# Optimization experiments

Measured on AMD Instinct MI355X. Metric: run time of the kernel, lower is better.

The kernel has to match this reference:

```python
import jax, jax.numpy as jnp
import numpy as np

B, S, IN_DIM = 8, 2048, 8
EMB, HEADS, NCLS = 512, 8, 3
HDIM = EMB // HEADS
HALF = EMB // 2


def setup_inputs() -> dict:
    key = jax.random.key(0)
    ks = jax.random.split(key, 16)
    g = lambda k, shp, fan_in: jax.random.normal(k, shp, jnp.float32) / np.sqrt(fan_in)
    return {
        "features": jax.random.normal(ks[0], (B, S, IN_DIM), jnp.float32),
        "timestamps": jax.random.uniform(ks[1], (B, S, 1), jnp.float32),
        # FeatureEmbedding
        "Wf": g(ks[2], (IN_DIM, EMB), IN_DIM), "bf": jnp.zeros((EMB,), jnp.float32),
        # Time2Vec
        "Wl": g(ks[3], (1, HALF), 1), "bl": jnp.zeros((HALF,), jnp.float32),
        "Wp": g(ks[4], (1, HALF), 1), "bp": jnp.zeros((HALF,), jnp.float32),
        # TimeAwareAttention
        "Wq": g(ks[5], (EMB, EMB), EMB), "bq": jnp.zeros((EMB,), jnp.float32),
        "Wk": g(ks[6], (EMB, EMB), EMB), "bk": jnp.zeros((EMB,), jnp.float32),
        "Wv": g(ks[7], (EMB, EMB), EMB), "bv": jnp.zeros((EMB,), jnp.float32),
        "Wo": g(ks[8], (EMB, EMB), EMB), "bo": jnp.zeros((EMB,), jnp.float32),
        "time_decay": jnp.ones((1,), jnp.float32),
        # Classifier MLP (dropout is identity in eval)
        "W1": g(ks[9], (EMB, EMB // 2), EMB), "b1": jnp.zeros((EMB // 2,), jnp.float32),
        "W2": g(ks[10], (EMB // 2, NCLS), EMB // 2), "b2": jnp.zeros((NCLS,), jnp.float32),
    }


def reference(features, timestamps, Wf, bf, Wl, bl, Wp, bp,
              Wq, bq, Wk, bk, Wv, bv, Wo, bo, time_decay, W1, b1, W2, b2):
    # embeddings: feature linear + Time2Vec(linear || sin(linear))
    feat_emb = features @ Wf + bf                              # [B,S,E]
    time_emb = jnp.concatenate(
        [timestamps @ Wl + bl, jnp.sin(timestamps @ Wp + bp)], axis=-1)
    x = feat_emb + time_emb                                    # [B,S,E]

    # pairwise time-decay weights: exp(-decay * |t_i - t_j|)  [B,S,S]
    t = timestamps[..., 0]
    decay = jnp.exp(-time_decay[0] * jnp.abs(t[:, :, None] - t[:, None, :]))

    def split_heads(y):  # [B,S,E] -> [B,H,S,D]
        return y.reshape(B, S, HEADS, HDIM).transpose(0, 2, 1, 3)

    q = split_heads(x @ Wq + bq)
    k = split_heads(x @ Wk + bk)
    v = split_heads(x @ Wv + bv)

    scores = jnp.einsum('bhsd,bhtd->bhst', q, k) / np.sqrt(HDIM).astype(np.float32)
    scores = scores * decay[:, None, :, :]                     # elementwise decay bias
    attn = jax.nn.softmax(scores, axis=-1)
    out = jnp.einsum('bhst,bhtd->bhsd', attn, v)               # [B,H,S,D]
    out = out.transpose(0, 2, 1, 3).reshape(B, S, EMB)
    out = out @ Wo + bo

    h = out[:, -1, :]                                          # last token
    h = jax.nn.relu(h @ W1 + b1)
    logits = h @ W2 + b2                                       # [B,NCLS]
    return logits
```

## Files before the change

### kernel.cpp

```cpp
#include <hip/hip_runtime.h>
#include <hip/hip_bf16.h>
#include <math.h>

#define B 8
#define S 2048
#define IN_DIM 8
#define EMB 512
#define HEADS 8
#define HDIM 64
#define HALF 256
#define NCLS 3
#define NCHUNK 64
#define CT 32

#define WS_KQ    0
#define WS_COEF1 32768
#define WS_PM    33536
#define WS_PS    99072
#define WS_POP   1147648

__global__ __launch_bounds__(256) void k_head(
    const float* __restrict__ feat, const float* __restrict__ ts,
    const float* __restrict__ Wf, const float* __restrict__ bf,
    const float* __restrict__ Wl, const float* __restrict__ bl,
    const float* __restrict__ Wp, const float* __restrict__ bp,
    const float* __restrict__ Wq, const float* __restrict__ bq,
    const float* __restrict__ Wk, const float* __restrict__ bk,
    float* __restrict__ ws)
{
    const int h = blockIdx.x;
    const int b = blockIdx.y;
    const int bh = b*HEADS + h;
    const int tid = threadIdx.x;
    __shared__ float xl[EMB];
    __shared__ __align__(16) float qc[HDIM];
    __shared__ float kq[EMB];
    __shared__ float red[4][64];
    __shared__ float red10[4][12];

    {
        const float tl = ts[b*S + (S-1)];
        float fv[IN_DIM];
        #pragma unroll
        for (int i = 0; i < IN_DIM; ++i) fv[i] = feat[(b*S + (S-1))*IN_DIM + i];
        #pragma unroll
        for (int r = 0; r < 2; ++r) {
            const int e = tid + r*256;
            float acc = bf[e];
            #pragma unroll
            for (int i = 0; i < IN_DIM; ++i) acc += fv[i]*Wf[i*EMB + e];
            if (r == 0) acc += tl*Wl[e] + bl[e];
            else        acc += __sinf(tl*Wp[e-HALF] + bp[e-HALF]);
            xl[e] = acc;
        }
    }
    __syncthreads();
    {
        const int eo = tid & 63, jq = tid >> 6;
        float acc = (jq == 0) ? bq[h*HDIM + eo] : 0.f;
        #pragma unroll 8
        for (int j = jq*128; j < jq*128 + 128; ++j)
            acc += xl[j]*Wq[j*EMB + h*HDIM + eo];
        red[jq][eo] = acc;
    }
    __syncthreads();
    if (tid < HDIM) qc[tid] = red[0][tid]+red[1][tid]+red[2][tid]+red[3][tid];
    __syncthreads();
    {
        #pragma unroll
        for (int r = 0; r < 2; ++r) {
            const int j = tid + r*256;
            const float4* wr = (const float4*)(Wk + j*EMB + h*HDIM);
            const float4* qv = (const float4*)qc;
            float acc = 0.f;
            #pragma unroll
            for (int k = 0; k < 16; ++k) {
                const float4 w = wr[k], q4 = qv[k];
                acc += w.x*q4.x + w.y*q4.y + w.z*q4.z + w.w*q4.w;
            }
            kq[j] = acc;
            if (j >= HALF) ws[WS_KQ + bh*EMB + j] = acc;
        }
    }
    __syncthreads();
    {
        float a[IN_DIM] = {0.f,0.f,0.f,0.f,0.f,0.f,0.f,0.f};
        float c0 = 0.f, c1 = 0.f;
        #pragma unroll
        for (int r = 0; r < 2; ++r) {
            const int e = tid + r*256;
            const float kv = kq[e];
            #pragma unroll
            for (int i = 0; i < IN_DIM; ++i) a[i] += Wf[i*EMB + e]*kv;
            c0 += bf[e]*kv;
            if (r == 0) { c0 += bl[e]*kv; c1 += Wl[e]*kv; }
        }
        if (tid < HDIM) c0 += qc[tid]*bk[h*HDIM + tid];
        #pragma unroll
        for (int off = 32; off >= 1; off >>= 1) {
            #pragma unroll
            for (int i = 0; i < IN_DIM; ++i) a[i] += __shfl_xor(a[i], off, 64);
            c0 += __shfl_xor(c0, off, 64);
            c1 += __shfl_xor(c1, off, 64);
        }
        const int wid = tid >> 6, lane = tid & 63;
        if (lane == 0) {
            #pragma unroll
            for (int i = 0; i < IN_DIM; ++i) red10[wid][i] = a[i];
            red10[wid][8] = c0; red10[wid][9] = c1;
        }
        __syncthreads();
        if (tid < 10)
            ws[WS_COEF1 + bh*12 + tid] =
                red10[0][tid]+red10[1][tid]+red10[2][tid]+red10[3][tid];
    }
}

__global__ __launch_bounds__(256) void k_part(
    const float* __restrict__ feat, const float* __restrict__ ts,
    const float* __restrict__ Wp, const float* __restrict__ bp,
    const float* __restrict__ tdp, float* __restrict__ ws)
{
    const int c = blockIdx.x;
    const int b = blockIdx.y;
    const int tid = threadIdx.x;
    const int t0 = c*CT;

    __shared__ float sin_l[256*33];
    __shared__ __align__(16) float kqh[HEADS][256];
    __shared__ __align__(16) float w_l[CT*8];
    __shared__ float tv_l[CT];
    __shared__ float f_l[CT*9];
    __shared__ float cf[96];

    if (tid < CT) tv_l[tid] = ts[b*S + t0 + tid];
    for (int idx = tid; idx < CT*IN_DIM; idx += 256) {
        const int tt = idx >> 3, i = idx & 7;
        f_l[tt*9 + i] = feat[(b*S + t0 + tt)*IN_DIM + i];
    }
    for (int idx = tid; idx < HEADS*256; idx += 256)
        ((float*)kqh)[idx] = ws[WS_KQ + (b*HEADS + (idx >> 8))*EMB + HALF + (idx & 255)];
    if (tid < 96) cf[tid] = ws[WS_COEF1 + b*96 + tid];
    const float tl = ts[b*S + (S-1)];
    const float td = tdp[0];
    __syncthreads();

    {
        const float wj = Wp[tid], bj = bp[tid];
        float* srow = sin_l + tid*33;
        #pragma unroll 4
        for (int tt = 0; tt < CT; ++tt)
            srow[tt] = __sinf(tv_l[tt]*wj + bj);
    }
    __syncthreads();

    const int t = tid & (CT-1), h = tid >> 5;
    const float tv = tv_l[t];
    float fv[IN_DIM];
    #pragma unroll
    for (int i = 0; i < IN_DIM; ++i) fv[i] = f_l[t*9 + i];
    const float dec = __expf(-td*fabsf(tl - tv));
    float sc;
    {
        float acc = 0.f;
        const float4* kq4 = (const float4*)&kqh[h][0];
        #pragma unroll 4
        for (int j4 = 0; j4 < 64; ++j4) {
            const float s0 = sin_l[(j4*4+0)*33 + t];
            const float s1 = sin_l[(j4*4+1)*33 + t];
            const float s2 = sin_l[(j4*4+2)*33 + t];
            const float s3 = sin_l[(j4*4+3)*33 + t];
            const float4 ka = kq4[j4];
            acc += s0*ka.x + s1*ka.y + s2*ka.z + s3*ka.w;
        }
        float base = cf[h*12+8] + tv*cf[h*12+9];
        #pragma unroll
        for (int i = 0; i < IN_DIM; ++i) base += fv[i]*cf[h*12+i];
        sc = (base + acc)*0.125f*dec;
    }
    {
        float m = sc;
        #pragma unroll
        for (int off = 16; off >= 1; off >>= 1) m = fmaxf(m, __shfl_xor(m, off, 64));
        const float w = __expf(sc - m);
        float Z = w, ta = w*tv;
        float fa[IN_DIM];
        #pragma unroll
        for (int i = 0; i < IN_DIM; ++i) fa[i] = w*fv[i];
        #pragma unroll
        for (int off = 16; off >= 1; off >>= 1) {
            Z  += __shfl_xor(Z,  off, 64);
            ta += __shfl_xor(ta, off, 64);
            #pragma unroll
            for (int i = 0; i < IN_DIM; ++i) fa[i] += __shfl_xor(fa[i], off, 64);
        }
        w_l[t*8 + h] = w;
        if (t == 0) {
            float* pm = ws + WS_PM + ((b*NCHUNK + c)*HEADS + h)*16;
            pm[0] = m; pm[1] = Z; pm[2] = ta;
            #pragma unroll
            for (int i = 0; i < IN_DIM; ++i) pm[3+i] = fa[i];
        }
    }
    __syncthreads();
    {
        const int j = tid;
        float accS[HEADS] = {0.f,0.f,0.f,0.f,0.f,0.f,0.f,0.f};
        const float4* wv4 = (const float4*)w_l;
        const float* scol = sin_l + j*33;
        #pragma unroll 4
        for (int tt = 0; tt < CT; ++tt) {
            const float sv = scol[tt];
            const float4 wa = wv4[tt*2], wb = wv4[tt*2+1];
            accS[0] += wa.x*sv; accS[1] += wa.y*sv; accS[2] += wa.z*sv; accS[3] += wa.w*sv;
            accS[4] += wb.x*sv; accS[5] += wb.y*sv; accS[6] += wb.z*sv; accS[7] += wb.w*sv;
        }
        const int base = WS_PS + ((b*NCHUNK + c)*HEADS)*256 + j;
        #pragma unroll
        for (int hh = 0; hh < HEADS; ++hh) ws[base + hh*256] = accS[hh];
    }
}

__global__ __launch_bounds__(256) void k_ohw(
    const float* __restrict__ Wf, const float* __restrict__ bf,
    const float* __restrict__ Wl, const float* __restrict__ bl,
    const float* __restrict__ Wv, const float* __restrict__ bv,
    const float* __restrict__ Wo, float* __restrict__ ws)
{
    const int h = blockIdx.x;
    const int b = blockIdx.y;
    const int tid = threadIdx.x;
    __shared__ float pmL[NCHUNK][12];
    __shared__ float al[NCHUNK];
    __shared__ float cfL[10];
    __shared__ float wx[EMB];
    __shared__ float red[4][64];
    __shared__ __align__(16) float oh_c[HDIM];

    for (int idx = tid; idx < NCHUNK*11; idx += 256) {
        const int c = idx / 11, k = idx % 11;
        pmL[c][k] = ws[WS_PM + ((b*NCHUNK + c)*HEADS + h)*16 + k];
    }
    __syncthreads();
    float m = pmL[0][0];
    #pragma unroll 8
    for (int c = 1; c < NCHUNK; ++c) m = fmaxf(m, pmL[c][0]);
    if (tid < NCHUNK) al[tid] = __expf(pmL[tid][0] - m);
    __syncthreads();
    float Z = 0.f;
    #pragma unroll 8
    for (int c = 0; c < NCHUNK; ++c) Z += al[c]*pmL[c][1];
    const float inv = 1.f/Z;
    if (tid < 9) {
        const int k = (tid == 8) ? 2 : 3 + tid;
        float acc = 0.f;
        #pragma unroll 8
        for (int c = 0; c < NCHUNK; ++c) acc += al[c]*pmL[c][k];
        cfL[(tid == 8) ? 8 : tid] = acc*inv;
    }
    __syncthreads();
    {
        const int j = tid;
        float acc = 0.f;
        #pragma unroll 8
        for (int c = 0; c < NCHUNK; ++c)
            acc += al[c]*ws[WS_PS + ((b*NCHUNK + c)*HEADS + h)*256 + j];
        float vh = bf[HALF + j] + acc*inv;
        float vl = bf[j] + cfL[8]*Wl[j] + bl[j];
        #pragma unroll
        for (int i = 0; i < IN_DIM; ++i) {
            vh += cfL[i]*Wf[i*EMB + HALF + j];
            vl += cfL[i]*Wf[i*EMB + j];
        }
        wx[j] = vl;
        wx[HALF + j] = vh;
    }
    __syncthreads();
    {
        const int eo = tid & 63, jq = tid >> 6;
        const int e = h*HDIM + eo;
        float acc = 0.f;
        #pragma unroll 8
        for (int j = jq*128; j < jq*128 + 128; ++j)
            acc += wx[j]*Wv[j*EMB + e];
        red[jq][eo] = acc;
    }
    __syncthreads();
    if (tid < 64)
        oh_c[tid] = red[0][tid]+red[1][tid]+red[2][tid]+red[3][tid] + bv[h*HDIM + tid];
    __syncthreads();
    {
        #pragma unroll
        for (int r = 0; r < 2; ++r) {
            const int e = tid + r*256;
            float acc = 0.f;
            #pragma unroll 8
            for (int d = 0; d < HDIM; ++d)
                acc += oh_c[d]*Wo[(h*HDIM + d)*EMB + e];
            ws[WS_POP + (b*HEADS + h)*EMB + e] = acc;
        }
    }
}

__global__ __launch_bounds__(1024) void k_tail2(
    const float* __restrict__ bo,
    const float* __restrict__ W1, const float* __restrict__ b1,
    const float* __restrict__ W2, const float* __restrict__ b2,
    const float* __restrict__ ws, float* __restrict__ out)
{
    const int b = blockIdx.x;
    const int tid = threadIdx.x;
    __shared__ float opL[EMB];
    __shared__ float red[4][HALF];
    __shared__ float hhL[HALF];
    __shared__ float red3[4][3];

    if (tid < EMB) {
        float acc = bo[tid];
        #pragma unroll
        for (int h = 0; h < HEADS; ++h)
            acc += ws[WS_POP + (b*HEADS + h)*EMB + tid];
        opL[tid] = acc;
    }
    __syncthreads();
    {
        const int mm = tid & 255, jq = tid >> 8;
        float acc = 0.f;
        #pragma unroll 8
        for (int j = jq*128; j < jq*128 + 128; ++j)
            acc += opL[j]*W1[j*HALF + mm];
        red[jq][mm] = acc;
    }
    __syncthreads();
    if (tid < HALF)
        hhL[tid] = fmaxf(red[0][tid]+red[1][tid]+red[2][tid]+red[3][tid] + b1[tid], 0.f);
    __syncthreads();
    if (tid < HALF) {
        const float hv = hhL[tid];
        float p0 = hv*W2[tid*NCLS + 0];
        float p1 = hv*W2[tid*NCLS + 1];
        float p2 = hv*W2[tid*NCLS + 2];
        #pragma unroll
        for (int off = 32; off >= 1; off >>= 1) {
            p0 += __shfl_xor(p0, off, 64);
            p1 += __shfl_xor(p1, off, 64);
            p2 += __shfl_xor(p2, off, 64);
        }
        const int wid = tid >> 6;
        if ((tid & 63) == 0) { red3[wid][0] = p0; red3[wid][1] = p1; red3[wid][2] = p2; }
    }
    __syncthreads();
    if (tid < NCLS)
        out[b*NCLS + tid] = red3[0][tid]+red3[1][tid]+red3[2][tid]+red3[3][tid] + b2[tid];
}

extern "C" void kernel_launch(void* const* d_in, const int* in_sizes, int n_in,
                              void* d_out, int out_size, void* d_ws, size_t ws_size,
                              hipStream_t stream)
{
    const float* feat = (const float*)d_in[0];
    const float* ts   = (const float*)d_in[1];
    const float* Wf = (const float*)d_in[2];
    const float* bf = (const float*)d_in[3];
    const float* Wl = (const float*)d_in[4];
    const float* bl = (const float*)d_in[5];
    const float* Wp = (const float*)d_in[6];
    const float* bp = (const float*)d_in[7];
    const float* Wq = (const float*)d_in[8];
    const float* bq = (const float*)d_in[9];
    const float* Wk = (const float*)d_in[10];
    const float* bk = (const float*)d_in[11];
    const float* Wv = (const float*)d_in[12];
    const float* bv = (const float*)d_in[13];
    const float* Wo = (const float*)d_in[14];
    const float* bo = (const float*)d_in[15];
    const float* td = (const float*)d_in[16];
    const float* W1 = (const float*)d_in[17];
    const float* b1 = (const float*)d_in[18];
    const float* W2 = (const float*)d_in[19];
    const float* b2 = (const float*)d_in[20];
    float* ws = (float*)d_ws;
    float* out = (float*)d_out;

    hipLaunchKernelGGL(k_head,  dim3(HEADS, B),  dim3(256),  0, stream,
                       feat, ts, Wf, bf, Wl, bl, Wp, bp, Wq, bq, Wk, bk, ws);
    hipLaunchKernelGGL(k_part,  dim3(NCHUNK, B), dim3(256),  0, stream,
                       feat, ts, Wp, bp, td, ws);
    hipLaunchKernelGGL(k_ohw,   dim3(HEADS, B),  dim3(256),  0, stream,
                       Wf, bf, Wl, bl, Wv, bv, Wo, ws);
    hipLaunchKernelGGL(k_tail2, dim3(B),         dim3(1024), 0, stream,
                       bo, W1, b1, W2, b2, ws, out);
}
```

Baseline: 48.59 us.

## Fuse output projection and classifier tail via last-block counter; double chunk size

The classifier tail kernel is merged into the per-head output kernel. Each block bumps an atomic per-batch counter, and the last of the eight head blocks reduces the partial Wo projections and runs the MLP. This removes one kernel launch and its dependency gap. The partial-softmax kernel now uses 64-token chunks with half as many chunks, each thread computing two heads. The sin table is stored row-major with padding so it can be read as float4. The counter relies on modulo-8 arithmetic, so it only works correctly if the workspace counter starts at a multiple of eight.

```diff
diff --git a/kernel.cpp b/kernel.cpp
--- a/kernel.cpp
+++ b/kernel.cpp
@@ -10,14 +10,16 @@
 #define HDIM 64
 #define HALF 256
 #define NCLS 3
-#define NCHUNK 64
-#define CT 32
+#define NCHUNK 32
+#define CT 64
+#define SINSTRIDE 260
 
 #define WS_KQ    0
 #define WS_COEF1 32768
 #define WS_PM    33536
-#define WS_PS    99072
-#define WS_POP   1147648
+#define WS_PS    66304
+#define WS_POP   590592
+#define WS_CTR   623360
 
 __global__ __launch_bounds__(256) void k_head(
     const float* __restrict__ feat, const float* __restrict__ ts,
@@ -126,7 +128,7 @@
     const int tid = threadIdx.x;
     const int t0 = c*CT;
 
-    __shared__ float sin_l[256*33];
+    __shared__ __align__(16) float sin_l[CT*SINSTRIDE];
     __shared__ __align__(16) float kqh[HEADS][256];
     __shared__ __align__(16) float w_l[CT*8];
     __shared__ float tv_l[CT];
@@ -147,48 +149,53 @@
 
     {
         const float wj = Wp[tid], bj = bp[tid];
-        float* srow = sin_l + tid*33;
         #pragma unroll 4
         for (int tt = 0; tt < CT; ++tt)
-            srow[tt] = __sinf(tv_l[tt]*wj + bj);
-    }
-    __syncthreads();
-
-    const int t = tid & (CT-1), h = tid >> 5;
+            sin_l[tt*SINSTRIDE + tid] = __sinf(tv_l[tt]*wj + bj);
+    }
+    __syncthreads();
+
+    const int t = tid & 63, h0 = tid >> 6;
     const float tv = tv_l[t];
     float fv[IN_DIM];
     #pragma unroll
     for (int i = 0; i < IN_DIM; ++i) fv[i] = f_l[t*9 + i];
     const float dec = __expf(-td*fabsf(tl - tv));
-    float sc;
-    {
-        float acc = 0.f;
-        const float4* kq4 = (const float4*)&kqh[h][0];
+    float sc[2];
+    {
+        float acc0 = 0.f, acc1 = 0.f;
+        const float4* srow = (const float4*)(sin_l + t*SINSTRIDE);
+        const float4* kq0 = (const float4*)&kqh[h0][0];
+        const float4* kq1 = (const float4*)&kqh[h0+4][0];
         #pragma unroll 4
         for (int j4 = 0; j4 < 64; ++j4) {
-            const float s0 = sin_l[(j4*4+0)*33 + t];
-            const float s1 = sin_l[(j4*4+1)*33 + t];
-            const float s2 = sin_l[(j4*4+2)*33 + t];
-            const float s3 = sin_l[(j4*4+3)*33 + t];
-            const float4 ka = kq4[j4];
-            acc += s0*ka.x + s1*ka.y + s2*ka.z + s3*ka.w;
-        }
-        float base = cf[h*12+8] + tv*cf[h*12+9];
-        #pragma unroll
-        for (int i = 0; i < IN_DIM; ++i) base += fv[i]*cf[h*12+i];
-        sc = (base + acc)*0.125f*dec;
-    }
-    {
-        float m = sc;
-        #pragma unroll
-        for (int off = 16; off >= 1; off >>= 1) m = fmaxf(m, __shfl_xor(m, off, 64));
-        const float w = __expf(sc - m);
+            const float4 sv = srow[j4];
+            const float4 ka = kq0[j4], kb = kq1[j4];
+            acc0 += sv.x*ka.x + sv.y*ka.y + sv.z*ka.z + sv.w*ka.w;
+            acc1 += sv.x*kb.x + sv.y*kb.y + sv.z*kb.z + sv.w*kb.w;
+        }
+        #pragma unroll
+        for (int p = 0; p < 2; ++p) {
+            const int h = h0 + p*4;
+            float base = cf[h*12+8] + tv*cf[h*12+9];
+            #pragma unroll
+            for (int i = 0; i < IN_DIM; ++i) base += fv[i]*cf[h*12+i];
+            sc[p] = (base + ((p == 0) ? acc0 : acc1))*0.125f*dec;
+        }
+    }
+    #pragma unroll
+    for (int p = 0; p < 2; ++p) {
+        const int h = h0 + p*4;
+        float m = sc[p];
+        #pragma unroll
+        for (int off = 32; off >= 1; off >>= 1) m = fmaxf(m, __shfl_xor(m, off, 64));
+        const float w = __expf(sc[p] - m);
         float Z = w, ta = w*tv;
         float fa[IN_DIM];
         #pragma unroll
         for (int i = 0; i < IN_DIM; ++i) fa[i] = w*fv[i];
         #pragma unroll
-        for (int off = 16; off >= 1; off >>= 1) {
+        for (int off = 32; off >= 1; off >>= 1) {
             Z  += __shfl_xor(Z,  off, 64);
             ta += __shfl_xor(ta, off, 64);
             #pragma unroll
@@ -207,25 +214,27 @@
         const int j = tid;
         float accS[HEADS] = {0.f,0.f,0.f,0.f,0.f,0.f,0.f,0.f};
         const float4* wv4 = (const float4*)w_l;
-        const float* scol = sin_l + j*33;
         #pragma unroll 4
         for (int tt = 0; tt < CT; ++tt) {
-            const float sv = scol[tt];
+            const float sv = sin_l[tt*SINSTRIDE + j];
             const float4 wa = wv4[tt*2], wb = wv4[tt*2+1];
             accS[0] += wa.x*sv; accS[1] += wa.y*sv; accS[2] += wa.z*sv; accS[3] += wa.w*sv;
             accS[4] += wb.x*sv; accS[5] += wb.y*sv; accS[6] += wb.z*sv; accS[7] += wb.w*sv;
         }
         const int base = WS_PS + ((b*NCHUNK + c)*HEADS)*256 + j;
         #pragma unroll
-        for (int hh = 0; hh < HEADS; ++hh) ws[base + hh*256] = accS[hh];
+        for (int h = 0; h < HEADS; ++h) ws[base + h*256] = accS[h];
     }
 }
 
-__global__ __launch_bounds__(256) void k_ohw(
+__global__ __launch_bounds__(512) void k_owt(
     const float* __restrict__ Wf, const float* __restrict__ bf,
     const float* __restrict__ Wl, const float* __restrict__ bl,
     const float* __restrict__ Wv, const float* __restrict__ bv,
-    const float* __restrict__ Wo, float* __restrict__ ws)
+    const float* __restrict__ Wo, const float* __restrict__ bo,
+    const float* __restrict__ W1, const float* __restrict__ b1,
+    const float* __restrict__ W2, const float* __restrict__ b2,
+    float* __restrict__ ws, float* __restrict__ out)
 {
     const int h = blockIdx.x;
     const int b = blockIdx.y;
@@ -234,13 +243,14 @@
     __shared__ float al[NCHUNK];
     __shared__ float cfL[10];
     __shared__ float wx[EMB];
-    __shared__ float red[4][64];
+    __shared__ float red[8][64];
     __shared__ __align__(16) float oh_c[HDIM];
-
-    for (int idx = tid; idx < NCHUNK*11; idx += 256) {
-        const int c = idx / 11, k = idx % 11;
-        pmL[c][k] = ws[WS_PM + ((b*NCHUNK + c)*HEADS + h)*16 + k];
-    }
+    __shared__ float hhL[HALF];
+    __shared__ float red3[4][3];
+    __shared__ unsigned tick;
+
+    if (tid < NCHUNK*11)
+        pmL[tid/11][tid%11] = ws[WS_PM + ((b*NCHUNK + tid/11)*HEADS + h)*16 + tid%11];
     __syncthreads();
     float m = pmL[0][0];
     #pragma unroll 8
@@ -260,20 +270,21 @@
     }
     __syncthreads();
     {
-        const int j = tid;
-        float acc = 0.f;
-        #pragma unroll 8
-        for (int c = 0; c < NCHUNK; ++c)
-            acc += al[c]*ws[WS_PS + ((b*NCHUNK + c)*HEADS + h)*256 + j];
-        float vh = bf[HALF + j] + acc*inv;
-        float vl = bf[j] + cfL[8]*Wl[j] + bl[j];
-        #pragma unroll
-        for (int i = 0; i < IN_DIM; ++i) {
-            vh += cfL[i]*Wf[i*EMB + HALF + j];
-            vl += cfL[i]*Wf[i*EMB + j];
-        }
-        wx[j] = vl;
-        wx[HALF + j] = vh;
+        const int e = tid;
+        float val = bf[e];
+        #pragma unroll
+        for (int i = 0; i < IN_DIM; ++i) val += cfL[i]*Wf[i*EMB + e];
+        if (e < HALF) {
+            val += cfL[8]*Wl[e] + bl[e];
+        } else {
+            const int j = e - HALF;
+            float acc = 0.f;
+            #pragma unroll 8
+            for (int c = 0; c < NCHUNK; ++c)
+                acc += al[c]*ws[WS_PS + ((b*NCHUNK + c)*HEADS + h)*256 + j];
+            val += acc*inv;
+        }
+        wx[e] = val;
     }
     __syncthreads();
     {
@@ -281,59 +292,58 @@
         const int e = h*HDIM + eo;
         float acc = 0.f;
         #pragma unroll 8
-        for (int j = jq*128; j < jq*128 + 128; ++j)
+        for (int j = jq*64; j < jq*64 + 64; ++j)
             acc += wx[j]*Wv[j*EMB + e];
         red[jq][eo] = acc;
     }
     __syncthreads();
-    if (tid < 64)
-        oh_c[tid] = red[0][tid]+red[1][tid]+red[2][tid]+red[3][tid] + bv[h*HDIM + tid];
-    __syncthreads();
-    {
-        #pragma unroll
-        for (int r = 0; r < 2; ++r) {
-            const int e = tid + r*256;
-            float acc = 0.f;
-            #pragma unroll 8
-            for (int d = 0; d < HDIM; ++d)
-                acc += oh_c[d]*Wo[(h*HDIM + d)*EMB + e];
-            ws[WS_POP + (b*HEADS + h)*EMB + e] = acc;
-        }
-    }
-}
-
-__global__ __launch_bounds__(1024) void k_tail2(
-    const float* __restrict__ bo,
-    const float* __restrict__ W1, const float* __restrict__ b1,
-    const float* __restrict__ W2, const float* __restrict__ b2,
-    const float* __restrict__ ws, float* __restrict__ out)
-{
-    const int b = blockIdx.x;
-    const int tid = threadIdx.x;
-    __shared__ float opL[EMB];
-    __shared__ float red[4][HALF];
-    __shared__ float hhL[HALF];
-    __shared__ float red3[4][3];
-
-    if (tid < EMB) {
-        float acc = bo[tid];
-        #pragma unroll
-        for (int h = 0; h < HEADS; ++h)
-            acc += ws[WS_POP + (b*HEADS + h)*EMB + tid];
-        opL[tid] = acc;
-    }
-    __syncthreads();
-    {
+    if (tid < 64) {
+        float s = 0.f;
+        #pragma unroll
+        for (int q = 0; q < 8; ++q) s += red[q][tid];
+        oh_c[tid] = s + bv[h*HDIM + tid];
+    }
+    __syncthreads();
+    {
+        const int e = tid;
+        float acc = 0.f;
+        #pragma unroll 8
+        for (int d = 0; d < HDIM; ++d)
+            acc += oh_c[d]*Wo[(h*HDIM + d)*EMB + e];
+        ws[WS_POP + (b*HEADS + h)*EMB + e] = acc;
+    }
+    __threadfence();
+    if (tid == 0) {
+        unsigned* ctr = (unsigned*)(ws + WS_CTR);
+        tick = atomicAdd(&ctr[b], 1u);
+    }
+    __syncthreads();
+    if ((tick & 7u) != 7u) return;
+    __threadfence();
+
+    {
+        const int e = tid;
+        float acc = bo[e];
+        #pragma unroll
+        for (int hh = 0; hh < HEADS; ++hh)
+            acc += ws[WS_POP + (b*HEADS + hh)*EMB + e];
+        wx[e] = acc;
+    }
+    __syncthreads();
+    {
+        float* redW1 = (float*)red;
         const int mm = tid & 255, jq = tid >> 8;
         float acc = 0.f;
         #pragma unroll 8
-        for (int j = jq*128; j < jq*128 + 128; ++j)
-            acc += opL[j]*W1[j*HALF + mm];
-        red[jq][mm] = acc;
-    }
-    __syncthreads();
-    if (tid < HALF)
-        hhL[tid] = fmaxf(red[0][tid]+red[1][tid]+red[2][tid]+red[3][tid] + b1[tid], 0.f);
+        for (int j = jq*256; j < jq*256 + 256; ++j)
+            acc += wx[j]*W1[j*HALF + mm];
+        redW1[jq*HALF + mm] = acc;
+    }
+    __syncthreads();
+    if (tid < HALF) {
+        const float* redW1 = (const float*)red;
+        hhL[tid] = fmaxf(redW1[tid] + redW1[HALF + tid] + b1[tid], 0.f);
+    }
     __syncthreads();
     if (tid < HALF) {
         const float hv = hhL[tid];
@@ -382,12 +392,10 @@
     float* ws = (float*)d_ws;
     float* out = (float*)d_out;
 
-    hipLaunchKernelGGL(k_head,  dim3(HEADS, B),  dim3(256),  0, stream,
+    hipLaunchKernelGGL(k_head, dim3(HEADS, B),  dim3(256), 0, stream,
                        feat, ts, Wf, bf, Wl, bl, Wp, bp, Wq, bq, Wk, bk, ws);
-    hipLaunchKernelGGL(k_part,  dim3(NCHUNK, B), dim3(256),  0, stream,
+    hipLaunchKernelGGL(k_part, dim3(NCHUNK, B), dim3(256), 0, stream,
                        feat, ts, Wp, bp, td, ws);
-    hipLaunchKernelGGL(k_ohw,   dim3(HEADS, B),  dim3(256),  0, stream,
-                       Wf, bf, Wl, bl, Wv, bv, Wo, ws);
-    hipLaunchKernelGGL(k_tail2, dim3(B),         dim3(1024), 0, stream,
-                       bo, W1, b1, W2, b2, ws, out);
+    hipLaunchKernelGGL(k_owt,  dim3(HEADS, B),  dim3(512), 0, stream,
+                       Wf, bf, Wl, bl, Wv, bv, Wo, bo, W1, b1, W2, b2, ws, out);
 }
```

After: 53.88 us. +10.9%, slower.
